# Kernel tuning notes

Hardware: AMD Instinct MI355X
Metric: run time of the kernel (lower is better)

## Reference

```python
import jax, jax.numpy as jnp
import numpy as np

B, H, S, D = 2, 16, 2048, 64

def setup_inputs() -> dict:
    key = jax.random.key(0)
    kq, kk, kv = jax.random.split(key, 3)
    Q = jax.random.normal(kq, (B, H, S, D), dtype=jnp.float32)
    K = jax.random.normal(kk, (B, H, S, D), dtype=jnp.float32)
    V = jax.random.normal(kv, (B, H, S, D), dtype=jnp.float32)
    # causal mask, broadcastable over batch and heads
    mask = jnp.tril(jnp.ones((S, S), dtype=bool))[None, None, :, :]
    return {"Q": Q, "K": K, "V": V, "mask": mask}

def reference(Q, K, V, mask):
    # scores: [B,H,S,S]
    scores = jnp.einsum('bhqd,bhkd->bhqk', Q, K)
    # original applies mask (-inf) BEFORE scaling; -inf/scale == -inf so math matches
    scores = jnp.where(mask, scores, -jnp.inf)
    scores = scores / jnp.sqrt(jnp.float32(K.shape[-1]))
    attn = jax.nn.softmax(scores, axis=-1)
    return jnp.einsum('bhqk,bhkd->bhqd', attn, V)
```

## Files before the change

kernel.cpp:

```cpp
#include <hip/hip_runtime.h>

#define SEQ 2048
#define HD  64
#define SCALE 0.18033688011111772f

typedef __bf16 bf16x8 __attribute__((ext_vector_type(8)));
typedef __bf16 bf16x2 __attribute__((ext_vector_type(2)));
typedef float  f32x4  __attribute__((ext_vector_type(4)));
typedef float  f32x16 __attribute__((ext_vector_type(16)));

#define BAR_LGKM() asm volatile("s_waitcnt lgkmcnt(0)\n\ts_barrier" ::: "memory")

union PU { unsigned u[4]; bf16x8 v; };

__device__ __forceinline__ unsigned pk2(float lo, float hi) {
    union { unsigned u; bf16x2 v; } t;
    t.v = bf16x2{(__bf16)lo, (__bf16)hi};
    return t.u;
}

__device__ __forceinline__ void plswap(unsigned &x, unsigned &y) {
#if __has_builtin(__builtin_amdgcn_permlane32_swap)
    auto r = __builtin_amdgcn_permlane32_swap(x, y, false, false);
    x = (unsigned)r[0];
    y = (unsigned)r[1];
#else
    asm("v_permlane32_swap_b32 %0, %1" : "+v"(x), "+v"(y));
#endif
}

__global__ __launch_bounds__(256, 4) void attn_fwd(
    const float* __restrict__ Q,
    const float* __restrict__ K,
    const float* __restrict__ V,
    float* __restrict__ O)
{
    __shared__ __align__(16) unsigned char smem[32768];
    #define KBp(kh,b,key,c8) ((__bf16*)(smem +         (((kh)<<13) + ((b)<<12) + ((key)<<7) + ((c8)<<4))))
    #define VTp(kh,b,r,c8)   ((__bf16*)(smem + 16384 + (((kh)<<13) + ((b)<<12) + ((r)<<6)   + ((c8)<<4))))

    const int tid   = threadIdx.x;
    const int wave  = tid >> 6;
    const int lane  = tid & 63;
    const int n     = lane & 31;
    const int p     = lane >> 5;
    const int strip = wave & 1;
    const int kh    = wave >> 1;

    const int x  = blockIdx.x;
    const int bh = x & 31;
    const int s  = x >> 5;
    const int q  = (s & 16) ? (31 - (s & 15)) : s;

    const int q0    = q * 64 + strip * 32;
    const int iters = q + 1;
    const int tS0   = kh * (q + 1);

    const float* __restrict__ Qh = Q + (size_t)bh * SEQ * HD;
    const float* __restrict__ Kh = K + (size_t)bh * SEQ * HD;
    const float* __restrict__ Vh = V + (size_t)bh * SEQ * HD;
    float* __restrict__       Oh = O + (size_t)bh * SEQ * HD;

    bf16x8 qf[4];
    {
        const float* qrow = Qh + (size_t)(q0 + n) * HD;
        #pragma unroll
        for (int c = 0; c < 4; ++c) {
            f32x4 a = *(const f32x4*)(qrow + 16 * c + 8 * p);
            f32x4 b = *(const f32x4*)(qrow + 16 * c + 8 * p + 4);
            #pragma unroll
            for (int j = 0; j < 4; ++j) {
                qf[c][j]     = (__bf16)(a[j] * SCALE);
                qf[c][4 + j] = (__bf16)(b[j] * SCALE);
            }
        }
    }

    f32x16 oT[2] = {};
    float  l_own = 0.f;

    const int local = tid & 127;
    const int key_s = local >> 2;
    const int dgi   = local & 3;
    const int Ls    = local & 31;
    const int ko    = local >> 5;
    const int swk   = key_s & 7;
    const int swv   = Ls & 3;

    const float* kbase = Kh + (size_t)key_s * HD + dgi * 16;
    const float* vbase = Vh + (size_t)(ko * 8) * HD + 2 * Ls;

    f32x4  kst[4];
    float2 vst[8];

    auto loadt = [&](int t) {
        const size_t off = (size_t)(32 * t) * HD;
        const float* kp = kbase + off;
        #pragma unroll
        for (int j = 0; j < 4; ++j) kst[j] = *(const f32x4*)(kp + 4 * j);
        const float* vp = vbase + off;
        #pragma unroll
        for (int j = 0; j < 8; ++j) vst[j] = *(const float2*)(vp + (size_t)j * HD);
    };

    auto stage = [&](int nb) {
        bf16x8 w0, w1;
        #pragma unroll
        for (int j = 0; j < 4; ++j) {
            w0[j] = (__bf16)kst[0][j]; w0[4 + j] = (__bf16)kst[1][j];
            w1[j] = (__bf16)kst[2][j]; w1[4 + j] = (__bf16)kst[3][j];
        }
        *(bf16x8*)KBp(kh, nb, key_s, (2 * dgi)     ^ swk) = w0;
        *(bf16x8*)KBp(kh, nb, key_s, (2 * dgi + 1) ^ swk) = w1;

        bf16x8 v0, v1;
        #pragma unroll
        for (int j = 0; j < 8; ++j) { v0[j] = (__bf16)vst[j].x; v1[j] = (__bf16)vst[j].y; }
        *(bf16x8*)VTp(kh, nb, 2 * Ls,     ko ^ swv) = v0;
        *(bf16x8*)VTp(kh, nb, 2 * Ls + 1, ko ^ swv) = v1;
    };

    loadt(tS0);
    stage(0);
    if (iters > 1) loadt(tS0 + 1);

    for (int i = 0; i < iters; ++i) {
        BAR_LGKM();
        const int cur = i & 1;

        if (!kh || (i < q + strip)) {
            __builtin_amdgcn_s_setprio(1);
            f32x16 sT = {};
            #pragma unroll
            for (int cc = 0; cc < 4; ++cc) {
                bf16x8 kf = *(const bf16x8*)KBp(kh, cur, n, (2 * cc + p) ^ (n & 7));
                sT = __builtin_amdgcn_mfma_f32_32x32x16_bf16(kf, qf[cc], sT, 0, 0, 0);
            }

            const int  T    = tS0 + i;
            const bool diag = (T == 2 * q + strip);

            float pv[16];
            float ts = 0.f;
            #pragma unroll
            for (int r = 0; r < 16; ++r) {
                float pe = __builtin_amdgcn_exp2f(sT[r]);
                if (diag) {
                    const int kk = (r & 3) + 8 * (r >> 2) + 4 * p;
                    pe = (kk <= n) ? pe : 0.f;
                }
                pv[r] = pe;
                ts += pe;
            }
            l_own += ts;

            unsigned a0 = pk2(pv[0],  pv[1]),  a1 = pk2(pv[2],  pv[3]);
            unsigned a2 = pk2(pv[4],  pv[5]),  a3 = pk2(pv[6],  pv[7]);
            unsigned b0 = pk2(pv[8],  pv[9]),  b1 = pk2(pv[10], pv[11]);
            unsigned b2 = pk2(pv[12], pv[13]), b3 = pk2(pv[14], pv[15]);
            plswap(a0, a2);
            plswap(a1, a3);
            plswap(b0, b2);
            plswap(b1, b3);
            PU pu0, pu1;
            pu0.u[0] = a0; pu0.u[1] = a1; pu0.u[2] = a2; pu0.u[3] = a3;
            pu1.u[0] = b0; pu1.u[1] = b1; pu1.u[2] = b2; pu1.u[3] = b3;
            bf16x8 pf0 = pu0.v;
            bf16x8 pf1 = pu1.v;

            const int swn = (n >> 1) & 3;
            #pragma unroll
            for (int dg = 0; dg < 2; ++dg) {
                bf16x8 vf0 = *(const bf16x8*)VTp(kh, cur, 32 * dg + n, p ^ swn);
                bf16x8 vf1 = *(const bf16x8*)VTp(kh, cur, 32 * dg + n, (2 + p) ^ swn);
                oT[dg] = __builtin_amdgcn_mfma_f32_32x32x16_bf16(vf0, pf0, oT[dg], 0, 0, 0);
                oT[dg] = __builtin_amdgcn_mfma_f32_32x32x16_bf16(vf1, pf1, oT[dg], 0, 0, 0);
            }
            __builtin_amdgcn_s_setprio(0);
        }

        if (i + 1 < iters) stage(cur ^ 1);
        if (i + 2 < iters) loadt(tS0 + i + 2);
    }

    __syncthreads();
    float* Os = (float*)smem;
    const int cb = strip * 2112;
    float l_part = l_own + __shfl_xor(l_own, 32, 64);

    if (kh == 1) {
        #pragma unroll
        for (int dg = 0; dg < 2; ++dg)
            #pragma unroll
            for (int r = 0; r < 16; ++r)
                Os[cb + (dg * 16 + r) * 64 + lane] = oT[dg][r];
        Os[cb + 2048 + lane] = l_part;
    }
    __syncthreads();
    if (kh == 0) {
        const float linv = 1.0f / (l_part + Os[cb + 2048 + lane]);
        #pragma unroll
        for (int dg = 0; dg < 2; ++dg) {
            #pragma unroll
            for (int u = 0; u < 4; ++u) {
                f32x4 o;
                #pragma unroll
                for (int j = 0; j < 4; ++j) {
                    const int r = 4 * u + j;
                    o[j] = (oT[dg][r] + Os[cb + (dg * 16 + r) * 64 + lane]) * linv;
                }
                *(f32x4*)&Oh[(size_t)(q0 + n) * HD + dg * 32 + u * 8 + 4 * p] = o;
            }
        }
    }
}

extern "C" void kernel_launch(void* const* d_in, const int* in_sizes, int n_in,
                              void* d_out, int out_size, void* d_ws, size_t ws_size,
                              hipStream_t stream) {
    const float* Q = (const float*)d_in[0];
    const float* K = (const float*)d_in[1];
    const float* V = (const float*)d_in[2];
    float* O = (float*)d_out;

    dim3 grid(1024);
    dim3 block(256);
    attn_fwd<<<grid, block, 0, stream>>>(Q, K, V, O);
}
```

Before: 132.2 us.

## Split KV tiles across four waves with paired query tiles per block

Each block now processes two 32-row query tiles (u and 63-u) in sequence, which balances causal work across blocks. Within a tile, the four waves split the KV tiles round-robin, each using a private LDS region, so no block barrier is needed per KV step. The partial outputs and row sums are then reduced through LDS by one wave. This drops the double-buffered register prefetch and the per-iteration barriers, but global load latency is no longer overlapped inside a wave and the final reduction does more LDS traffic.

```diff
diff --git a/kernel.cpp b/kernel.cpp
--- a/kernel.cpp
+++ b/kernel.cpp
@@ -8,8 +8,6 @@
 typedef __bf16 bf16x2 __attribute__((ext_vector_type(2)));
 typedef float  f32x4  __attribute__((ext_vector_type(4)));
 typedef float  f32x16 __attribute__((ext_vector_type(16)));
-
-#define BAR_LGKM() asm volatile("s_waitcnt lgkmcnt(0)\n\ts_barrier" ::: "memory")
 
 union PU { unsigned u[4]; bf16x8 v; };
 
@@ -36,110 +34,94 @@
     float* __restrict__ O)
 {
     __shared__ __align__(16) unsigned char smem[32768];
-    #define KBp(kh,b,key,c8) ((__bf16*)(smem +         (((kh)<<13) + ((b)<<12) + ((key)<<7) + ((c8)<<4))))
-    #define VTp(kh,b,r,c8)   ((__bf16*)(smem + 16384 + (((kh)<<13) + ((b)<<12) + ((r)<<6)   + ((c8)<<4))))
-
-    const int tid   = threadIdx.x;
-    const int wave  = tid >> 6;
-    const int lane  = tid & 63;
-    const int n     = lane & 31;
-    const int p     = lane >> 5;
-    const int strip = wave & 1;
-    const int kh    = wave >> 1;
+    #define KBw(w,key,c8) ((__bf16*)(smem + ((w)<<13) +        (((key)<<7) + ((c8)<<4))))
+    #define VTw(w,r,c8)   ((__bf16*)(smem + ((w)<<13) + 4096 + (((r)<<6)   + ((c8)<<4))))
+    #define OSw(w)        ((float*)(smem + (w)*8448))
+
+    const int tid  = threadIdx.x;
+    const int wave = tid >> 6;
+    const int lane = tid & 63;
+    const int n    = lane & 31;
+    const int p    = lane >> 5;
 
     const int x  = blockIdx.x;
     const int bh = x & 31;
-    const int s  = x >> 5;
-    const int q  = (s & 16) ? (31 - (s & 15)) : s;
-
-    const int q0    = q * 64 + strip * 32;
-    const int iters = q + 1;
-    const int tS0   = kh * (q + 1);
+    const int pu = x >> 5;
 
     const float* __restrict__ Qh = Q + (size_t)bh * SEQ * HD;
     const float* __restrict__ Kh = K + (size_t)bh * SEQ * HD;
     const float* __restrict__ Vh = V + (size_t)bh * SEQ * HD;
     float* __restrict__       Oh = O + (size_t)bh * SEQ * HD;
 
-    bf16x8 qf[4];
-    {
-        const float* qrow = Qh + (size_t)(q0 + n) * HD;
-        #pragma unroll
-        for (int c = 0; c < 4; ++c) {
-            f32x4 a = *(const f32x4*)(qrow + 16 * c + 8 * p);
-            f32x4 b = *(const f32x4*)(qrow + 16 * c + 8 * p + 4);
-            #pragma unroll
-            for (int j = 0; j < 4; ++j) {
-                qf[c][j]     = (__bf16)(a[j] * SCALE);
-                qf[c][4 + j] = (__bf16)(b[j] * SCALE);
-            }
-        }
-    }
-
-    f32x16 oT[2] = {};
-    float  l_own = 0.f;
-
-    const int local = tid & 127;
-    const int key_s = local >> 2;
-    const int dgi   = local & 3;
-    const int Ls    = local & 31;
-    const int ko    = local >> 5;
-    const int swk   = key_s & 7;
-    const int swv   = Ls & 3;
-
-    const float* kbase = Kh + (size_t)key_s * HD + dgi * 16;
-    const float* vbase = Vh + (size_t)(ko * 8) * HD + 2 * Ls;
-
-    f32x4  kst[4];
-    float2 vst[8];
-
-    auto loadt = [&](int t) {
-        const size_t off = (size_t)(32 * t) * HD;
-        const float* kp = kbase + off;
-        #pragma unroll
-        for (int j = 0; j < 4; ++j) kst[j] = *(const f32x4*)(kp + 4 * j);
-        const float* vp = vbase + off;
-        #pragma unroll
-        for (int j = 0; j < 8; ++j) vst[j] = *(const float2*)(vp + (size_t)j * HD);
-    };
-
-    auto stage = [&](int nb) {
-        bf16x8 w0, w1;
-        #pragma unroll
-        for (int j = 0; j < 4; ++j) {
-            w0[j] = (__bf16)kst[0][j]; w0[4 + j] = (__bf16)kst[1][j];
-            w1[j] = (__bf16)kst[2][j]; w1[4 + j] = (__bf16)kst[3][j];
-        }
-        *(bf16x8*)KBp(kh, nb, key_s, (2 * dgi)     ^ swk) = w0;
-        *(bf16x8*)KBp(kh, nb, key_s, (2 * dgi + 1) ^ swk) = w1;
-
-        bf16x8 v0, v1;
-        #pragma unroll
-        for (int j = 0; j < 8; ++j) { v0[j] = (__bf16)vst[j].x; v1[j] = (__bf16)vst[j].y; }
-        *(bf16x8*)VTp(kh, nb, 2 * Ls,     ko ^ swv) = v0;
-        *(bf16x8*)VTp(kh, nb, 2 * Ls + 1, ko ^ swv) = v1;
-    };
-
-    loadt(tS0);
-    stage(0);
-    if (iters > 1) loadt(tS0 + 1);
-
-    for (int i = 0; i < iters; ++i) {
-        BAR_LGKM();
-        const int cur = i & 1;
-
-        if (!kh || (i < q + strip)) {
+    #pragma unroll 1
+    for (int half = 0; half < 2; ++half) {
+        const int u  = half ? (63 - pu) : pu;
+        const int R0 = u * 32;
+        const int nt = u + 1;
+
+        bf16x8 qf[4];
+        {
+            const float* qrow = Qh + (size_t)(R0 + n) * HD;
+            #pragma unroll
+            for (int c = 0; c < 4; ++c) {
+                f32x4 a = *(const f32x4*)(qrow + 16 * c + 8 * p);
+                f32x4 b = *(const f32x4*)(qrow + 16 * c + 8 * p + 4);
+                #pragma unroll
+                for (int j = 0; j < 4; ++j) {
+                    qf[c][j]     = (__bf16)(a[j] * SCALE);
+                    qf[c][4 + j] = (__bf16)(b[j] * SCALE);
+                }
+            }
+        }
+
+        f32x16 oT[2] = {};
+        float  l_own = 0.f;
+
+        #pragma unroll 1
+        for (int T = wave; T < nt; T += 4) {
+            #pragma unroll
+            for (int t = 0; t < 2; ++t) {
+                const int local = lane + (t << 6);
+                const int key_s = local >> 2;
+                const int dgi   = local & 3;
+                const int swk   = key_s & 7;
+                const float* kp = Kh + (size_t)(32 * T + key_s) * HD + dgi * 16;
+                f32x4 k0 = *(const f32x4*)(kp);
+                f32x4 k1 = *(const f32x4*)(kp + 4);
+                f32x4 k2 = *(const f32x4*)(kp + 8);
+                f32x4 k3 = *(const f32x4*)(kp + 12);
+                bf16x8 w0, w1;
+                #pragma unroll
+                for (int j = 0; j < 4; ++j) {
+                    w0[j] = (__bf16)k0[j]; w0[4 + j] = (__bf16)k1[j];
+                    w1[j] = (__bf16)k2[j]; w1[4 + j] = (__bf16)k3[j];
+                }
+                *(bf16x8*)KBw(wave, key_s, (2 * dgi)     ^ swk) = w0;
+                *(bf16x8*)KBw(wave, key_s, (2 * dgi + 1) ^ swk) = w1;
+
+                const int Ls = local & 31;
+                const int ko = local >> 5;
+                const int swv = Ls & 3;
+                const float* vp = Vh + (size_t)(32 * T + 8 * ko) * HD + 2 * Ls;
+                float2 vv[8];
+                #pragma unroll
+                for (int j = 0; j < 8; ++j) vv[j] = *(const float2*)(vp + (size_t)j * HD);
+                bf16x8 v0, v1;
+                #pragma unroll
+                for (int j = 0; j < 8; ++j) { v0[j] = (__bf16)vv[j].x; v1[j] = (__bf16)vv[j].y; }
+                *(bf16x8*)VTw(wave, 2 * Ls,     ko ^ swv) = v0;
+                *(bf16x8*)VTw(wave, 2 * Ls + 1, ko ^ swv) = v1;
+            }
+
             __builtin_amdgcn_s_setprio(1);
             f32x16 sT = {};
             #pragma unroll
             for (int cc = 0; cc < 4; ++cc) {
-                bf16x8 kf = *(const bf16x8*)KBp(kh, cur, n, (2 * cc + p) ^ (n & 7));
+                bf16x8 kf = *(const bf16x8*)KBw(wave, n, (2 * cc + p) ^ (n & 7));
                 sT = __builtin_amdgcn_mfma_f32_32x32x16_bf16(kf, qf[cc], sT, 0, 0, 0);
             }
 
-            const int  T    = tS0 + i;
-            const bool diag = (T == 2 * q + strip);
-
+            const bool diag = (T == u);
             float pv[16];
             float ts = 0.f;
             #pragma unroll
@@ -171,47 +153,47 @@
             const int swn = (n >> 1) & 3;
             #pragma unroll
             for (int dg = 0; dg < 2; ++dg) {
-                bf16x8 vf0 = *(const bf16x8*)VTp(kh, cur, 32 * dg + n, p ^ swn);
-                bf16x8 vf1 = *(const bf16x8*)VTp(kh, cur, 32 * dg + n, (2 + p) ^ swn);
+                bf16x8 vf0 = *(const bf16x8*)VTw(wave, 32 * dg + n, p ^ swn);
+                bf16x8 vf1 = *(const bf16x8*)VTw(wave, 32 * dg + n, (2 + p) ^ swn);
                 oT[dg] = __builtin_amdgcn_mfma_f32_32x32x16_bf16(vf0, pf0, oT[dg], 0, 0, 0);
                 oT[dg] = __builtin_amdgcn_mfma_f32_32x32x16_bf16(vf1, pf1, oT[dg], 0, 0, 0);
             }
             __builtin_amdgcn_s_setprio(0);
         }
 
-        if (i + 1 < iters) stage(cur ^ 1);
-        if (i + 2 < iters) loadt(tS0 + i + 2);
-    }
-
-    __syncthreads();
-    float* Os = (float*)smem;
-    const int cb = strip * 2112;
-    float l_part = l_own + __shfl_xor(l_own, 32, 64);
-
-    if (kh == 1) {
-        #pragma unroll
-        for (int dg = 0; dg < 2; ++dg)
-            #pragma unroll
-            for (int r = 0; r < 16; ++r)
-                Os[cb + (dg * 16 + r) * 64 + lane] = oT[dg][r];
-        Os[cb + 2048 + lane] = l_part;
-    }
-    __syncthreads();
-    if (kh == 0) {
-        const float linv = 1.0f / (l_part + Os[cb + 2048 + lane]);
-        #pragma unroll
-        for (int dg = 0; dg < 2; ++dg) {
-            #pragma unroll
-            for (int u = 0; u < 4; ++u) {
-                f32x4 o;
-                #pragma unroll
-                for (int j = 0; j < 4; ++j) {
-                    const int r = 4 * u + j;
-                    o[j] = (oT[dg][r] + Os[cb + (dg * 16 + r) * 64 + lane]) * linv;
-                }
-                *(f32x4*)&Oh[(size_t)(q0 + n) * HD + dg * 32 + u * 8 + 4 * p] = o;
-            }
-        }
+        float l_part = l_own + __shfl_xor(l_own, 32, 64);
+
+        __syncthreads();
+        if (wave != 3) {
+            #pragma unroll
+            for (int dg = 0; dg < 2; ++dg)
+                #pragma unroll
+                for (int r = 0; r < 16; ++r)
+                    OSw(wave)[(dg * 16 + r) * 64 + lane] = oT[dg][r];
+            OSw(wave)[2048 + lane] = l_part;
+        }
+        __syncthreads();
+        if (wave == 3) {
+            const float lsum = l_part + OSw(0)[2048 + lane]
+                                      + OSw(1)[2048 + lane]
+                                      + OSw(2)[2048 + lane];
+            const float linv = 1.0f / lsum;
+            #pragma unroll
+            for (int dg = 0; dg < 2; ++dg) {
+                #pragma unroll
+                for (int u4 = 0; u4 < 4; ++u4) {
+                    f32x4 o;
+                    #pragma unroll
+                    for (int j = 0; j < 4; ++j) {
+                        const int r   = 4 * u4 + j;
+                        const int idx = (dg * 16 + r) * 64 + lane;
+                        o[j] = (oT[dg][r] + OSw(0)[idx] + OSw(1)[idx] + OSw(2)[idx]) * linv;
+                    }
+                    *(f32x4*)&Oh[(size_t)(R0 + n) * HD + dg * 32 + u4 * 8 + 4 * p] = o;
+                }
+            }
+        }
+        __syncthreads();
     }
 }
 
```

New measurement: 165.0 us. +24.8%, slower.

## Process two key tiles per barrier round with doubled register prefetch

Applied to the files above, without the earlier changes.

The main loop now handles two 32-key tiles per iteration. Both are staged into the two LDS buffers together, then computed back-to-back, so there are half as many outer iterations but two barriers per round. Global prefetch now holds two tiles in registers at once, which raises register use, so launch bounds drop from 4 to 3 blocks per CU. The aim is to cut barrier and synchronisation overhead per tile. The cost is lower occupancy and less overlap, because staging now happens between barriers and no longer runs behind compute.

```diff
diff --git a/kernel.cpp b/kernel.cpp
--- a/kernel.cpp
+++ b/kernel.cpp
@@ -29,7 +29,7 @@
 #endif
 }
 
-__global__ __launch_bounds__(256, 4) void attn_fwd(
+__global__ __launch_bounds__(256, 3) void attn_fwd(
     const float* __restrict__ Q,
     const float* __restrict__ K,
     const float* __restrict__ V,
@@ -52,9 +52,10 @@
     const int s  = x >> 5;
     const int q  = (s & 16) ? (31 - (s & 15)) : s;
 
-    const int q0    = q * 64 + strip * 32;
-    const int iters = q + 1;
-    const int tS0   = kh * (q + 1);
+    const int q0   = q * 64 + strip * 32;
+    const int nt   = q + 1;
+    const int jmax = (nt + 1) >> 1;
+    const int tS0  = kh * nt;
 
     const float* __restrict__ Qh = Q + (size_t)bh * SEQ * HD;
     const float* __restrict__ Kh = K + (size_t)bh * SEQ * HD;
@@ -90,97 +91,110 @@
     const float* kbase = Kh + (size_t)key_s * HD + dgi * 16;
     const float* vbase = Vh + (size_t)(ko * 8) * HD + 2 * Ls;
 
-    f32x4  kst[4];
-    float2 vst[8];
-
-    auto loadt = [&](int t) {
-        const size_t off = (size_t)(32 * t) * HD;
-        const float* kp = kbase + off;
-        #pragma unroll
-        for (int j = 0; j < 4; ++j) kst[j] = *(const f32x4*)(kp + 4 * j);
-        const float* vp = vbase + off;
-        #pragma unroll
-        for (int j = 0; j < 8; ++j) vst[j] = *(const float2*)(vp + (size_t)j * HD);
+    f32x4  kst[2][4];
+    float2 vst[2][8];
+
+    auto loadt = [&](int j) {
+        #pragma unroll
+        for (int t = 0; t < 2; ++t) {
+            const int s32 = 2 * j + t;
+            if (s32 < nt) {
+                const size_t off = (size_t)(32 * (tS0 + s32)) * HD;
+                const float* kp = kbase + off;
+                #pragma unroll
+                for (int jj = 0; jj < 4; ++jj) kst[t][jj] = *(const f32x4*)(kp + 4 * jj);
+                const float* vp = vbase + off;
+                #pragma unroll
+                for (int jj = 0; jj < 8; ++jj) vst[t][jj] = *(const float2*)(vp + (size_t)jj * HD);
+            }
+        }
     };
 
-    auto stage = [&](int nb) {
-        bf16x8 w0, w1;
-        #pragma unroll
-        for (int j = 0; j < 4; ++j) {
-            w0[j] = (__bf16)kst[0][j]; w0[4 + j] = (__bf16)kst[1][j];
-            w1[j] = (__bf16)kst[2][j]; w1[4 + j] = (__bf16)kst[3][j];
-        }
-        *(bf16x8*)KBp(kh, nb, key_s, (2 * dgi)     ^ swk) = w0;
-        *(bf16x8*)KBp(kh, nb, key_s, (2 * dgi + 1) ^ swk) = w1;
-
-        bf16x8 v0, v1;
-        #pragma unroll
-        for (int j = 0; j < 8; ++j) { v0[j] = (__bf16)vst[j].x; v1[j] = (__bf16)vst[j].y; }
-        *(bf16x8*)VTp(kh, nb, 2 * Ls,     ko ^ swv) = v0;
-        *(bf16x8*)VTp(kh, nb, 2 * Ls + 1, ko ^ swv) = v1;
+    auto stage = [&](int j) {
+        #pragma unroll
+        for (int t = 0; t < 2; ++t) {
+            const int s32 = 2 * j + t;
+            if (s32 < nt) {
+                bf16x8 w0, w1;
+                #pragma unroll
+                for (int jj = 0; jj < 4; ++jj) {
+                    w0[jj] = (__bf16)kst[t][0][jj]; w0[4 + jj] = (__bf16)kst[t][1][jj];
+                    w1[jj] = (__bf16)kst[t][2][jj]; w1[4 + jj] = (__bf16)kst[t][3][jj];
+                }
+                *(bf16x8*)KBp(kh, t, key_s, (2 * dgi)     ^ swk) = w0;
+                *(bf16x8*)KBp(kh, t, key_s, (2 * dgi + 1) ^ swk) = w1;
+
+                bf16x8 v0, v1;
+                #pragma unroll
+                for (int jj = 0; jj < 8; ++jj) { v0[jj] = (__bf16)vst[t][jj].x; v1[jj] = (__bf16)vst[t][jj].y; }
+                *(bf16x8*)VTp(kh, t, 2 * Ls,     ko ^ swv) = v0;
+                *(bf16x8*)VTp(kh, t, 2 * Ls + 1, ko ^ swv) = v1;
+            }
+        }
     };
 
-    loadt(tS0);
-    stage(0);
-    if (iters > 1) loadt(tS0 + 1);
-
-    for (int i = 0; i < iters; ++i) {
+    loadt(0);
+
+    #pragma unroll 1
+    for (int j = 0; j < jmax; ++j) {
         BAR_LGKM();
-        const int cur = i & 1;
-
-        if (!kh || (i < q + strip)) {
-            __builtin_amdgcn_s_setprio(1);
-            f32x16 sT = {};
-            #pragma unroll
-            for (int cc = 0; cc < 4; ++cc) {
-                bf16x8 kf = *(const bf16x8*)KBp(kh, cur, n, (2 * cc + p) ^ (n & 7));
-                sT = __builtin_amdgcn_mfma_f32_32x32x16_bf16(kf, qf[cc], sT, 0, 0, 0);
-            }
-
-            const int  T    = tS0 + i;
-            const bool diag = (T == 2 * q + strip);
-
-            float pv[16];
-            float ts = 0.f;
-            #pragma unroll
-            for (int r = 0; r < 16; ++r) {
-                float pe = __builtin_amdgcn_exp2f(sT[r]);
-                if (diag) {
-                    const int kk = (r & 3) + 8 * (r >> 2) + 4 * p;
-                    pe = (kk <= n) ? pe : 0.f;
-                }
-                pv[r] = pe;
-                ts += pe;
-            }
-            l_own += ts;
-
-            unsigned a0 = pk2(pv[0],  pv[1]),  a1 = pk2(pv[2],  pv[3]);
-            unsigned a2 = pk2(pv[4],  pv[5]),  a3 = pk2(pv[6],  pv[7]);
-            unsigned b0 = pk2(pv[8],  pv[9]),  b1 = pk2(pv[10], pv[11]);
-            unsigned b2 = pk2(pv[12], pv[13]), b3 = pk2(pv[14], pv[15]);
-            plswap(a0, a2);
-            plswap(a1, a3);
-            plswap(b0, b2);
-            plswap(b1, b3);
-            PU pu0, pu1;
-            pu0.u[0] = a0; pu0.u[1] = a1; pu0.u[2] = a2; pu0.u[3] = a3;
-            pu1.u[0] = b0; pu1.u[1] = b1; pu1.u[2] = b2; pu1.u[3] = b3;
-            bf16x8 pf0 = pu0.v;
-            bf16x8 pf1 = pu1.v;
-
-            const int swn = (n >> 1) & 3;
-            #pragma unroll
-            for (int dg = 0; dg < 2; ++dg) {
-                bf16x8 vf0 = *(const bf16x8*)VTp(kh, cur, 32 * dg + n, p ^ swn);
-                bf16x8 vf1 = *(const bf16x8*)VTp(kh, cur, 32 * dg + n, (2 + p) ^ swn);
-                oT[dg] = __builtin_amdgcn_mfma_f32_32x32x16_bf16(vf0, pf0, oT[dg], 0, 0, 0);
-                oT[dg] = __builtin_amdgcn_mfma_f32_32x32x16_bf16(vf1, pf1, oT[dg], 0, 0, 0);
-            }
-            __builtin_amdgcn_s_setprio(0);
-        }
-
-        if (i + 1 < iters) stage(cur ^ 1);
-        if (i + 2 < iters) loadt(tS0 + i + 2);
+
+        stage(j);
+        if (j + 1 < jmax) loadt(j + 1);
+
+        BAR_LGKM();
+
+        __builtin_amdgcn_s_setprio(1);
+        #pragma unroll
+        for (int b = 0; b < 2; ++b) {
+            const int i = 2 * j + b;
+            if (i < nt && (!kh || (i < q + strip))) {
+                f32x16 sT = {};
+                #pragma unroll
+                for (int cc = 0; cc < 4; ++cc) {
+                    bf16x8 kf = *(const bf16x8*)KBp(kh, b, n, (2 * cc + p) ^ (n & 7));
+                    sT = __builtin_amdgcn_mfma_f32_32x32x16_bf16(kf, qf[cc], sT, 0, 0, 0);
+                }
+
+                const bool diag = (tS0 + i == 2 * q + strip);
+                float ts = 0.f;
+                #pragma unroll
+                for (int r = 0; r < 16; ++r) {
+                    float pe = __builtin_amdgcn_exp2f(sT[r]);
+                    if (diag) {
+                        const int kk = (r & 3) + 8 * (r >> 2) + 4 * p;
+                        pe = (kk <= n) ? pe : 0.f;
+                    }
+                    sT[r] = pe;
+                    ts += pe;
+                }
+                l_own += ts;
+
+                unsigned a0 = pk2(sT[0],  sT[1]),  a1 = pk2(sT[2],  sT[3]);
+                unsigned a2 = pk2(sT[4],  sT[5]),  a3 = pk2(sT[6],  sT[7]);
+                unsigned b0 = pk2(sT[8],  sT[9]),  b1 = pk2(sT[10], sT[11]);
+                unsigned b2 = pk2(sT[12], sT[13]), b3 = pk2(sT[14], sT[15]);
+                plswap(a0, a2);
+                plswap(a1, a3);
+                plswap(b0, b2);
+                plswap(b1, b3);
+                PU pu0, pu1;
+                pu0.u[0] = a0; pu0.u[1] = a1; pu0.u[2] = a2; pu0.u[3] = a3;
+                pu1.u[0] = b0; pu1.u[1] = b1; pu1.u[2] = b2; pu1.u[3] = b3;
+                bf16x8 pf0 = pu0.v;
+                bf16x8 pf1 = pu1.v;
+
+                const int swn = (n >> 1) & 3;
+                #pragma unroll
+                for (int dg = 0; dg < 2; ++dg) {
+                    bf16x8 vf0 = *(const bf16x8*)VTp(kh, b, 32 * dg + n, p ^ swn);
+                    bf16x8 vf1 = *(const bf16x8*)VTp(kh, b, 32 * dg + n, (2 + p) ^ swn);
+                    oT[dg] = __builtin_amdgcn_mfma_f32_32x32x16_bf16(vf0, pf0, oT[dg], 0, 0, 0);
+                    oT[dg] = __builtin_amdgcn_mfma_f32_32x32x16_bf16(vf1, pf1, oT[dg], 0, 0, 0);
+                }
+            }
+        }
+        __builtin_amdgcn_s_setprio(0);
     }
 
     __syncthreads();
```

After: 135.2 us. 1.02x slower.

## Widen workgroup to 128 query rows with 8 waves sharing K/V tiles

Applied to the files above, without the earlier changes.

Each workgroup now handles 128 query rows (four 32-row strips) and two key halves using 512 threads, so every staged K/V tile in shared memory serves four query strips instead of two. The grid halves to 512 blocks, and the load/stage work per thread halves. The aim is to reduce global K/V traffic and conversion work per query row. The cost is coarser causal load balancing, with some waves idle on tiles beyond their diagonal, plus lower occupancy under launch bounds of 512 threads and 2 blocks.

```diff
diff --git a/kernel.cpp b/kernel.cpp
--- a/kernel.cpp
+++ b/kernel.cpp
@@ -5,6 +5,7 @@
 #define SCALE 0.18033688011111772f
 
 typedef __bf16 bf16x8 __attribute__((ext_vector_type(8)));
+typedef __bf16 bf16x4 __attribute__((ext_vector_type(4)));
 typedef __bf16 bf16x2 __attribute__((ext_vector_type(2)));
 typedef float  f32x4  __attribute__((ext_vector_type(4)));
 typedef float  f32x16 __attribute__((ext_vector_type(16)));
@@ -29,32 +30,33 @@
 #endif
 }
 
-__global__ __launch_bounds__(256, 4) void attn_fwd(
+__global__ __launch_bounds__(512, 2) void attn_fwd(
     const float* __restrict__ Q,
     const float* __restrict__ K,
     const float* __restrict__ V,
     float* __restrict__ O)
 {
-    __shared__ __align__(16) unsigned char smem[32768];
+    __shared__ __align__(16) unsigned char smem[33792];
     #define KBp(kh,b,key,c8) ((__bf16*)(smem +         (((kh)<<13) + ((b)<<12) + ((key)<<7) + ((c8)<<4))))
     #define VTp(kh,b,r,c8)   ((__bf16*)(smem + 16384 + (((kh)<<13) + ((b)<<12) + ((r)<<6)   + ((c8)<<4))))
 
-    const int tid   = threadIdx.x;
-    const int wave  = tid >> 6;
-    const int lane  = tid & 63;
-    const int n     = lane & 31;
-    const int p     = lane >> 5;
-    const int strip = wave & 1;
-    const int kh    = wave >> 1;
+    const int tid  = threadIdx.x;
+    const int wave = tid >> 6;
+    const int lane = tid & 63;
+    const int n    = lane & 31;
+    const int p    = lane >> 5;
+    const int w3   = wave & 3;
+    const int kh   = wave >> 2;
 
     const int x  = blockIdx.x;
     const int bh = x & 31;
-    const int s  = x >> 5;
-    const int q  = (s & 16) ? (31 - (s & 15)) : s;
-
-    const int q0    = q * 64 + strip * 32;
-    const int iters = q + 1;
-    const int tS0   = kh * (q + 1);
+    const int sr = x >> 5;
+    const int s  = (sr & 8) ? (15 - (sr & 7)) : sr;
+
+    const int R0   = s * 128 + w3 * 32;
+    const int span = 4 * s + w3;
+    const int jmax = 2 * s + 2;
+    const int tB   = kh * jmax;
 
     const float* __restrict__ Qh = Q + (size_t)bh * SEQ * HD;
     const float* __restrict__ Kh = K + (size_t)bh * SEQ * HD;
@@ -63,7 +65,7 @@
 
     bf16x8 qf[4];
     {
-        const float* qrow = Qh + (size_t)(q0 + n) * HD;
+        const float* qrow = Qh + (size_t)(R0 + n) * HD;
         #pragma unroll
         for (int c = 0; c < 4; ++c) {
             f32x4 a = *(const f32x4*)(qrow + 16 * c + 8 * p);
@@ -79,56 +81,57 @@
     f32x16 oT[2] = {};
     float  l_own = 0.f;
 
-    const int local = tid & 127;
-    const int key_s = local >> 2;
-    const int dgi   = local & 3;
-    const int Ls    = local & 31;
-    const int ko    = local >> 5;
+    const int sg    = tid >> 8;
+    const int t8    = tid & 255;
+    const int key_s = t8 >> 3;
+    const int dgi8  = t8 & 7;
     const int swk   = key_s & 7;
+    const int Ls    = t8 & 31;
+    const int ko    = t8 >> 5;
     const int swv   = Ls & 3;
-
-    const float* kbase = Kh + (size_t)key_s * HD + dgi * 16;
-    const float* vbase = Vh + (size_t)(ko * 8) * HD + 2 * Ls;
-
-    f32x4  kst[4];
-    float2 vst[8];
-
-    auto loadt = [&](int t) {
-        const size_t off = (size_t)(32 * t) * HD;
+    const int ku    = ko >> 1;
+    const int khalf = ko & 1;
+
+    const float* kbase = Kh + (size_t)key_s * HD + dgi8 * 8;
+    const float* vbase = Vh + (size_t)(ko * 4) * HD + 2 * Ls;
+
+    f32x4  kst[2];
+    float2 vst[4];
+
+    auto loadt = [&](int j) {
+        const size_t off = (size_t)(32 * (sg * jmax + j)) * HD;
         const float* kp = kbase + off;
-        #pragma unroll
-        for (int j = 0; j < 4; ++j) kst[j] = *(const f32x4*)(kp + 4 * j);
+        kst[0] = *(const f32x4*)(kp);
+        kst[1] = *(const f32x4*)(kp + 4);
         const float* vp = vbase + off;
         #pragma unroll
-        for (int j = 0; j < 8; ++j) vst[j] = *(const float2*)(vp + (size_t)j * HD);
+        for (int jj = 0; jj < 4; ++jj) vst[jj] = *(const float2*)(vp + (size_t)jj * HD);
     };
 
-    auto stage = [&](int nb) {
-        bf16x8 w0, w1;
-        #pragma unroll
-        for (int j = 0; j < 4; ++j) {
-            w0[j] = (__bf16)kst[0][j]; w0[4 + j] = (__bf16)kst[1][j];
-            w1[j] = (__bf16)kst[2][j]; w1[4 + j] = (__bf16)kst[3][j];
-        }
-        *(bf16x8*)KBp(kh, nb, key_s, (2 * dgi)     ^ swk) = w0;
-        *(bf16x8*)KBp(kh, nb, key_s, (2 * dgi + 1) ^ swk) = w1;
-
-        bf16x8 v0, v1;
-        #pragma unroll
-        for (int j = 0; j < 8; ++j) { v0[j] = (__bf16)vst[j].x; v1[j] = (__bf16)vst[j].y; }
-        *(bf16x8*)VTp(kh, nb, 2 * Ls,     ko ^ swv) = v0;
-        *(bf16x8*)VTp(kh, nb, 2 * Ls + 1, ko ^ swv) = v1;
+    auto stage = [&](int b) {
+        bf16x8 w0;
+        #pragma unroll
+        for (int j = 0; j < 4; ++j) { w0[j] = (__bf16)kst[0][j]; w0[4 + j] = (__bf16)kst[1][j]; }
+        *(bf16x8*)KBp(sg, b, key_s, dgi8 ^ swk) = w0;
+
+        bf16x4 v0, v1;
+        #pragma unroll
+        for (int j = 0; j < 4; ++j) { v0[j] = (__bf16)vst[j].x; v1[j] = (__bf16)vst[j].y; }
+        *(bf16x4*)(VTp(sg, b, 2 * Ls,     ku ^ swv) + 4 * khalf) = v0;
+        *(bf16x4*)(VTp(sg, b, 2 * Ls + 1, ku ^ swv) + 4 * khalf) = v1;
     };
 
-    loadt(tS0);
+    loadt(0);
     stage(0);
-    if (iters > 1) loadt(tS0 + 1);
-
-    for (int i = 0; i < iters; ++i) {
+    loadt(1);
+
+    #pragma unroll 1
+    for (int j = 0; j < jmax; ++j) {
         BAR_LGKM();
-        const int cur = i & 1;
-
-        if (!kh || (i < q + strip)) {
+        const int cur = j & 1;
+        const int T   = tB + j;
+
+        if (T <= span) {
             __builtin_amdgcn_s_setprio(1);
             f32x16 sT = {};
             #pragma unroll
@@ -137,10 +140,7 @@
                 sT = __builtin_amdgcn_mfma_f32_32x32x16_bf16(kf, qf[cc], sT, 0, 0, 0);
             }
 
-            const int  T    = tS0 + i;
-            const bool diag = (T == 2 * q + strip);
-
-            float pv[16];
+            const bool diag = (T == span);
             float ts = 0.f;
             #pragma unroll
             for (int r = 0; r < 16; ++r) {
@@ -149,15 +149,15 @@
                     const int kk = (r & 3) + 8 * (r >> 2) + 4 * p;
                     pe = (kk <= n) ? pe : 0.f;
                 }
-                pv[r] = pe;
+                sT[r] = pe;
                 ts += pe;
             }
             l_own += ts;
 
-            unsigned a0 = pk2(pv[0],  pv[1]),  a1 = pk2(pv[2],  pv[3]);
-            unsigned a2 = pk2(pv[4],  pv[5]),  a3 = pk2(pv[6],  pv[7]);
-            unsigned b0 = pk2(pv[8],  pv[9]),  b1 = pk2(pv[10], pv[11]);
-            unsigned b2 = pk2(pv[12], pv[13]), b3 = pk2(pv[14], pv[15]);
+            unsigned a0 = pk2(sT[0],  sT[1]),  a1 = pk2(sT[2],  sT[3]);
+            unsigned a2 = pk2(sT[4],  sT[5]),  a3 = pk2(sT[6],  sT[7]);
+            unsigned b0 = pk2(sT[8],  sT[9]),  b1 = pk2(sT[10], sT[11]);
+            unsigned b2 = pk2(sT[12], sT[13]), b3 = pk2(sT[14], sT[15]);
             plswap(a0, a2);
             plswap(a1, a3);
             plswap(b0, b2);
@@ -179,14 +179,15 @@
             __builtin_amdgcn_s_setprio(0);
         }
 
-        if (i + 1 < iters) stage(cur ^ 1);
-        if (i + 2 < iters) loadt(tS0 + i + 2);
-    }
+        if (j + 1 < jmax) stage(cur ^ 1);
+        if (j + 2 < jmax) loadt(j + 2);
+    }
+
+    float l_part = l_own + __shfl_xor(l_own, 32, 64);
 
     __syncthreads();
     float* Os = (float*)smem;
-    const int cb = strip * 2112;
-    float l_part = l_own + __shfl_xor(l_own, 32, 64);
+    const int cb = w3 * 2112;
 
     if (kh == 1) {
         #pragma unroll
@@ -202,14 +203,14 @@
         #pragma unroll
         for (int dg = 0; dg < 2; ++dg) {
             #pragma unroll
-            for (int u = 0; u < 4; ++u) {
+            for (int u4 = 0; u4 < 4; ++u4) {
                 f32x4 o;
                 #pragma unroll
                 for (int j = 0; j < 4; ++j) {
-                    const int r = 4 * u + j;
+                    const int r = 4 * u4 + j;
                     o[j] = (oT[dg][r] + Os[cb + (dg * 16 + r) * 64 + lane]) * linv;
                 }
-                *(f32x4*)&Oh[(size_t)(q0 + n) * HD + dg * 32 + u * 8 + 4 * p] = o;
+                *(f32x4*)&Oh[(size_t)(R0 + n) * HD + dg * 32 + u4 * 8 + 4 * p] = o;
             }
         }
     }
@@ -223,7 +224,7 @@
     const float* V = (const float*)d_in[2];
     float* O = (float*)d_out;
 
-    dim3 grid(1024);
-    dim3 block(256);
+    dim3 grid(512);
+    dim3 block(512);
     attn_fwd<<<grid, block, 0, stream>>>(Q, K, V, O);
 }
```

After: 125.4 us. 1.05x faster.
